# Kernel optimization log

Hardware: AMD Instinct MI355X
Metric: run time of the kernel (lower is better)

The kernel has to match this reference:

```python
import jax, jax.numpy as jnp
import numpy as np

B, T_ENC, T_DEC = 16, 256, 200
E, ATT, PRE, H, MEL, LOC, K = 512, 128, 256, 1024, 80, 32, 31


def setup_inputs() -> dict:
    key = jax.random.key(0)
    ks = jax.random.split(key, 20)
    s = lambda k, shape: jax.random.normal(k, shape, jnp.float32) * 0.02
    return dict(
        encoder_output=jax.random.normal(ks[0], (B, T_ENC, E), jnp.float32),
        padded_mels=jax.random.normal(ks[1], (B, T_DEC, MEL), jnp.float32),
        enc_proj_w=s(ks[2], (ATT, E)),
        lstm_proj_w=s(ks[3], (ATT, H)),
        loc_conv_w=s(ks[4], (LOC, 1, K)),
        loc_conv_b=jnp.zeros((LOC,), jnp.float32),
        loc_dense_w=s(ks[5], (ATT, LOC)),
        loc_dense_b=jnp.zeros((ATT,), jnp.float32),
        e_w=s(ks[6], (1, ATT)),
        e_b=jnp.zeros((1,), jnp.float32),
        prenet1_w=s(ks[7], (PRE, MEL)),
        prenet2_w=s(ks[8], (PRE, PRE)),
        w_ih0=s(ks[9], (4 * H, PRE + E)),
        w_hh0=s(ks[10], (4 * H, H)),
        b_ih0=jnp.zeros((4 * H,), jnp.float32),
        b_hh0=jnp.zeros((4 * H,), jnp.float32),
        w_ih1=s(ks[11], (4 * H, H)),
        w_hh1=s(ks[12], (4 * H, H)),
        b_ih1=jnp.zeros((4 * H,), jnp.float32),
        b_hh1=jnp.zeros((4 * H,), jnp.float32),
        proj_w=s(ks[13], (MEL, H + E)),
        proj_b=jnp.zeros((MEL,), jnp.float32),
        stop_w=s(ks[14], (1, H + E)),
        stop_b=jnp.zeros((1,), jnp.float32),
        text_lengths=jax.random.randint(ks[15], (B,), T_ENC // 2, T_ENC + 1),
    )


def _lstm_cell_zero(x, w_ih, b_ih, b_hh):
    # PyTorch LSTM cell with zero initial (h, c): h_prev contributes nothing
    # except the recurrent bias b_hh. Gate order: i, f, g, o.
    g = x @ w_ih.T + b_ih + b_hh
    i, f, gg, o = jnp.split(g, 4, axis=-1)
    c = jax.nn.sigmoid(i) * jnp.tanh(gg)  # f * c_prev == 0
    return jax.nn.sigmoid(o) * jnp.tanh(c)


def reference(encoder_output, padded_mels, enc_proj_w, lstm_proj_w, loc_conv_w,
              loc_conv_b, loc_dense_w, loc_dense_b, e_w, e_b, prenet1_w,
              prenet2_w, w_ih0, w_hh0, b_ih0, b_hh0, w_ih1, w_hh1, b_ih1,
              b_hh1, proj_w, proj_b, stop_w, stop_b, text_lengths):
    b, t_enc, _ = encoder_output.shape
    n_mel = padded_mels.shape[-1]
    h = w_hh0.shape[-1]
    pad = (loc_conv_w.shape[-1] - 1) // 2
    proc_enc = encoder_output @ enc_proj_w.T              # [B,Te,128]
    mask = jnp.arange(t_enc)[None, :] < text_lengths[:, None]
    # teacher forcing (ratio=1.0): prev mel at step t is padded_mels[:, t-1]
    prev_mels = jnp.concatenate(
        [jnp.zeros((b, 1, n_mel), padded_mels.dtype), padded_mels[:, :-1]],
        axis=1).transpose(1, 0, 2)                        # [Td,B,80]

    def step(carry, prev_mel):
        awc, h2 = carry                                   # [B,Te], [B,1024]
        # prenet (dropout omitted for a deterministic reference)
        x = jax.nn.relu(prev_mel @ prenet1_w.T)
        x = jax.nn.relu(x @ prenet2_w.T)                  # [B,256]
        # location-sensitive attention
        q = h2 @ lstm_proj_w.T                            # [B,128]
        loc = jax.lax.conv_general_dilated(
            awc[:, None, :], loc_conv_w, (1,), [(pad, pad)],
            dimension_numbers=('NCH', 'OIH', 'NCH')) + loc_conv_b[None, :, None]
        loc = jnp.einsum('bct,ac->bta', loc, loc_dense_w) + loc_dense_b
        en = jnp.tanh(q[:, None, :] + loc + proc_enc) @ e_w[0] + e_b[0]
        en = jnp.where(mask, en, -1e9)
        aw = jax.nn.softmax(en, axis=-1)                  # [B,Te]
        ctx = jnp.einsum('bt,bte->be', aw, encoder_output)  # [B,512]
        # 2-layer LSTM, state reset to zero every step (as in the original)
        li = jnp.concatenate([x, ctx], axis=-1)           # [B,768]
        h1 = _lstm_cell_zero(li, w_ih0, b_ih0, b_hh0)
        h2n = _lstm_cell_zero(h1, w_ih1, b_ih1, b_hh1)
        dec = jnp.concatenate([h2n, ctx], axis=-1)        # [B,1536]
        mel = dec @ proj_w.T + proj_b                     # [B,80]
        stop = (dec @ stop_w.T + stop_b)[:, 0]            # [B]
        return (awc + aw, h2n), (mel, stop)

    init = (jnp.zeros((b, t_enc), encoder_output.dtype),
            jnp.zeros((b, h), encoder_output.dtype))
    _, (mels, stops) = jax.lax.scan(step, init, prev_mels)
    return mels.transpose(1, 0, 2), stops.T               # [B,Td,80], [B,Td]
```

## Files before the change

kernel.cpp:

```cpp
#include <hip/hip_runtime.h>
#include <math.h>

#define NB   16
#define TE   256
#define TD   200
#define EE   512
#define ATT  128
#define PREN 256
#define HH   1024
#define NMEL 80
#define NLOC 32
#define KWW  31
#define PADW 15

#define OFF_X2   0
#define OFF_PE   (OFF_X2 + TD*NB*PREN)
#define OFF_AWC  (OFF_PE + NB*TE*ATT)
#define OFF_EN   (OFF_AWC + NB*TE)
#define OFF_Q    (OFF_EN + NB*TE)
#define OFF_CTX  (OFF_Q + NB*ATT)
#define OFF_H1   (OFF_CTX + NB*EE)
#define OFF_H2   (OFF_H1 + NB*HH)
#define OFF_BAR  (OFF_H2 + NB*HH)
#define BAR_U32  8192

#define ARR_G  0
#define ARR_L  4096

#define LW0_F4   (12*192)
#define LW1_F4   (12*256)
#define DYN_BYTES ((LW0_F4 + LW1_F4) * 16)

typedef float f4 __attribute__((ext_vector_type(4)));

__device__ __forceinline__ float sigmf(float x) { return 1.0f / (1.0f + expf(-x)); }
__device__ __forceinline__ float dot4(f4 a, f4 b) {
  return a.x*b.x + a.y*b.y + a.z*b.z + a.w*b.w;
}
__device__ __forceinline__ float red32(float v) {
  v += __shfl_down(v, 16, 32); v += __shfl_down(v, 8, 32);
  v += __shfl_down(v, 4, 32);  v += __shfl_down(v, 2, 32);
  v += __shfl_down(v, 1, 32);
  return v;
}

__device__ __forceinline__ unsigned ld_cg_u32(const unsigned* p) {
  unsigned r;
  asm volatile("global_load_dword %0, %1, off sc0 sc1\n\ts_waitcnt vmcnt(0)"
               : "=v"(r) : "v"(p) : "memory");
  return r;
}
__device__ __forceinline__ void st_cg_u32(unsigned* p, unsigned v) {
  asm volatile("global_store_dword %0, %1, off sc0 sc1" :: "v"(p), "v"(v) : "memory");
}
__device__ __forceinline__ float ld_cg_f32(const float* p) {
  float r;
  asm volatile("global_load_dword %0, %1, off sc0 sc1\n\ts_waitcnt vmcnt(0)"
               : "=v"(r) : "v"(p) : "memory");
  return r;
}
__device__ __forceinline__ void st_cg_f32(float* p, float v) {
  asm volatile("global_store_dword %0, %1, off sc0 sc1" :: "v"(p), "v"(v) : "memory");
}
__device__ __forceinline__ f4 ld_cg_f4(const f4* p) {
  f4 r;
  asm volatile("global_load_dwordx4 %0, %1, off sc0 sc1\n\ts_waitcnt vmcnt(0)"
               : "=v"(r) : "v"(p) : "memory");
  return r;
}
__device__ __forceinline__ void st_cg_f4(f4* p, f4 v) {
  asm volatile("global_store_dwordx4 %0, %1, off sc0 sc1" :: "v"(p), "v"(v) : "memory");
}
__device__ __forceinline__ void ld4_cg(f4& r0, f4& r1, f4& r2, f4& r3,
                                       const f4* a0, const f4* a1,
                                       const f4* a2, const f4* a3) {
  asm volatile(
    "global_load_dwordx4 %0, %4, off sc0 sc1\n\t"
    "global_load_dwordx4 %1, %5, off sc0 sc1\n\t"
    "global_load_dwordx4 %2, %6, off sc0 sc1\n\t"
    "global_load_dwordx4 %3, %7, off sc0 sc1\n\t"
    "s_waitcnt vmcnt(0)"
    : "=&v"(r0), "=&v"(r1), "=&v"(r2), "=&v"(r3)
    : "v"(a0), "v"(a1), "v"(a2), "v"(a3)
    : "memory");
}
__device__ __forceinline__ void ld8_cg(f4& r0, f4& r1, f4& r2, f4& r3,
                                       f4& r4, f4& r5, f4& r6, f4& r7,
                                       const f4* a0, const f4* a1, const f4* a2,
                                       const f4* a3, const f4* a4, const f4* a5,
                                       const f4* a6, const f4* a7) {
  asm volatile(
    "global_load_dwordx4 %0, %8, off sc0 sc1\n\t"
    "global_load_dwordx4 %1, %9, off sc0 sc1\n\t"
    "global_load_dwordx4 %2, %10, off sc0 sc1\n\t"
    "global_load_dwordx4 %3, %11, off sc0 sc1\n\t"
    "global_load_dwordx4 %4, %12, off sc0 sc1\n\t"
    "global_load_dwordx4 %5, %13, off sc0 sc1\n\t"
    "global_load_dwordx4 %6, %14, off sc0 sc1\n\t"
    "global_load_dwordx4 %7, %15, off sc0 sc1\n\t"
    "s_waitcnt vmcnt(0)"
    : "=&v"(r0), "=&v"(r1), "=&v"(r2), "=&v"(r3),
      "=&v"(r4), "=&v"(r5), "=&v"(r6), "=&v"(r7)
    : "v"(a0), "v"(a1), "v"(a2), "v"(a3),
      "v"(a4), "v"(a5), "v"(a6), "v"(a7)
    : "memory");
}

__device__ __forceinline__ void g_arrive(unsigned* bar, unsigned e) {
  __syncthreads();
  if (threadIdx.x == 0) st_cg_u32(bar + ARR_G + blockIdx.x * 16, e);
}
__device__ __forceinline__ void g_wait(unsigned* bar, unsigned e) {
  if (threadIdx.x < 256) {
    while (ld_cg_u32(bar + ARR_G + threadIdx.x * 16) < e) {}
  }
  __syncthreads();
}
__device__ __forceinline__ void l_arrive(unsigned* bar, unsigned e) {
  __syncthreads();
  if (threadIdx.x == 0) st_cg_u32(bar + ARR_L + blockIdx.x * 16, e);
}
__device__ __forceinline__ void l_wait(unsigned* bar, unsigned e, int b_grp) {
  if (threadIdx.x < 16) {
    while (ld_cg_u32(bar + ARR_L + (threadIdx.x * 16 + b_grp) * 16) < e) {}
  }
  __syncthreads();
}

__global__ void k_init(float* __restrict__ ws) {
  const int tid = threadIdx.x;
  float* awc = ws + OFF_AWC;
  float* qv  = ws + OFF_Q;
  unsigned* bar = (unsigned*)(ws + OFF_BAR);
  for (int i = tid; i < NB*TE; i += 256) st_cg_f32(awc + i, 0.0f);
  for (int i = tid; i < NB*ATT; i += 256) st_cg_f32(qv + i, 0.0f);
  for (int i = tid; i < BAR_U32; i += 256) st_cg_u32(bar + i, 0u);
}

__global__ void k_prenet(const float* __restrict__ mels,
                         const float* __restrict__ w1,
                         const float* __restrict__ w2,
                         float* __restrict__ x2) {
  const int t = blockIdx.x >> 4;
  const int b = blockIdx.x & 15;
  const int j = threadIdx.x;
  __shared__ float s_in[NMEL];
  __shared__ float s_x1[PREN];
  if (j < NMEL) s_in[j] = (t == 0) ? 0.0f : mels[(b*TD + (t-1))*NMEL + j];
  __syncthreads();
  float a1 = 0.0f;
  #pragma unroll 8
  for (int k = 0; k < NMEL; ++k) a1 += s_in[k] * w1[j*NMEL + k];
  s_x1[j] = fmaxf(a1, 0.0f);
  __syncthreads();
  float a2 = 0.0f;
  #pragma unroll 8
  for (int k = 0; k < PREN; ++k) a2 += s_x1[k] * w2[j*PREN + k];
  x2[(t*NB + b)*PREN + j] = fmaxf(a2, 0.0f);
}

__global__ void k_procenc(const float* __restrict__ enc,
                          const float* __restrict__ w,
                          float* __restrict__ pe) {
  const int bt = blockIdx.x;
  const int a = threadIdx.x;
  __shared__ float s_e[EE];
  for (int k = a; k < EE; k += 128) s_e[k] = enc[bt*EE + k];
  __syncthreads();
  float acc = 0.0f;
  #pragma unroll 8
  for (int k = 0; k < EE; ++k) acc += s_e[k] * w[a*EE + k];
  pe[bt*ATT + a] = acc;
}

__global__ void __launch_bounds__(512, 1) k_main(
    const float* __restrict__ enc,
    const float* __restrict__ lstm_proj_w,
    const float* __restrict__ loc_conv_w,
    const float* __restrict__ loc_conv_b,
    const float* __restrict__ loc_dense_w,
    const float* __restrict__ loc_dense_b,
    const float* __restrict__ e_w,
    const float* __restrict__ e_b,
    const float* __restrict__ w_ih0,
    const float* __restrict__ b_ih0,
    const float* __restrict__ b_hh0,
    const float* __restrict__ w_ih1,
    const float* __restrict__ b_ih1,
    const float* __restrict__ b_hh1,
    const float* __restrict__ proj_w,
    const float* __restrict__ proj_b,
    const float* __restrict__ stop_w,
    const float* __restrict__ stop_b,
    const int*   __restrict__ text_len,
    float* __restrict__ ws,
    float* __restrict__ out) {
  const int bid = blockIdx.x;
  const int tid = threadIdx.x;

  float* x2  = ws + OFF_X2;
  float* pe  = ws + OFF_PE;
  float* awc = ws + OFF_AWC;
  float* en  = ws + OFF_EN;
  float* qv  = ws + OFF_Q;
  float* ctx = ws + OFF_CTX;
  float* h1  = ws + OFF_H1;
  float* h2  = ws + OFF_H2;
  unsigned* bar = (unsigned*)(ws + OFF_BAR);

  __shared__ __align__(16) float s_ldw[NLOC*ATT];
  __shared__ float s_awc[64];
  __shared__ float s_loc[16*33];
  __shared__ float s_red[16];
  __shared__ float s_aw[256];
  __shared__ __align__(16) float s_dec[HH+EE];
  __shared__ float s_b0[12], s_b1[12];
  extern __shared__ __align__(16) float dynlds[];
  f4* lw0 = (f4*)dynlds;
  f4* lw1 = ((f4*)dynlds) + LW0_F4;

  const int b_grp = bid & 15;
  const int sub   = bid >> 4;
  const int h0    = bid * 4;

  for (int i = tid; i < NLOC*ATT; i += 512) {
    int c = i >> 7, a = i & 127;
    s_ldw[i] = loc_dense_w[a*NLOC + c];
  }
  if (tid < 12) {
    int g = tid >> 2, h = tid & 3;
    int gr = (g == 0 ? 0 : (g == 1 ? 2048 : 3072)) + h0 + h;
    s_b0[tid] = b_ih0[gr] + b_hh0[gr];
    s_b1[tid] = b_ih1[gr] + b_hh1[gr];
  }
  {
    const f4* w0_4 = (const f4*)w_ih0;
    const f4* w1_4 = (const f4*)w_ih1;
    for (int i = tid; i < LW0_F4; i += 512) {
      int r = i / 192, c = i - r*192;
      int g = r >> 2, h = r & 3;
      int grow = (g == 0 ? 0 : (g == 1 ? 2048 : 3072)) + h0 + h;
      lw0[i] = w0_4[grow*192 + c];
    }
    for (int i = tid; i < LW1_F4; i += 512) {
      int r = i >> 8, c = i & 255;
      int g = r >> 2, h = r & 3;
      int grow = (g == 0 ? 0 : (g == 1 ? 2048 : 3072)) + h0 + h;
      lw1[i] = w1_4[grow*256 + c];
    }
  }
  const int   lenb = text_len[b_grp];
  const float eb0  = e_b[0];

  const int tl = tid >> 5;
  const int j  = tid & 31;
  float lcw_r[KWW];
  #pragma unroll
  for (int k = 0; k < KWW; ++k) lcw_r[k] = loc_conv_w[j*KWW + k];
  const float lcb_r = loc_conv_b[j];
  const f4 db_r = *(const f4*)(loc_dense_b + 4*j);
  const f4 ew_r = *(const f4*)(e_w + 4*j);
  const f4 pe_r = *(const f4*)(pe + (size_t)(b_grp*TE + sub*16 + tl)*ATT + 4*j);
  const f4 ps_r = pe_r + db_r;
  const int e4i = tid >> 6;
  const int ts  = tid & 63;
  f4 encr[4];
  {
    const f4* enc4 = (const f4*)(enc + (size_t)b_grp*TE*EE);
    #pragma unroll
    for (int i = 0; i < 4; ++i)
      encr[i] = enc4[(size_t)(ts + 64*i)*(EE/4) + sub*8 + e4i];
  }
  const int pb = tid >> 5;
  const int kc = tid & 31;
  __syncthreads();

  unsigned eg = 0, el = 0;

  for (int t = 0; t < TD; ++t) {
    f4 pre;
    {
      if (tid >= 128 && tid < 176) {
        const int i = tid - 128;
        const int g = sub*16 - PADW + i;
        s_awc[i] = (i < 46 && g >= 0 && g < TE) ? ld_cg_f32(awc + b_grp*TE + g)
                                                : 0.0f;
      }
      __syncthreads();
      float cv = lcb_r;
      #pragma unroll
      for (int k = 0; k < KWW; ++k) cv += s_awc[tl + k] * lcw_r[k];
      s_loc[tl*33 + j] = cv;
      __syncthreads();
      f4 d4 = (f4){0.f, 0.f, 0.f, 0.f};
      #pragma unroll 8
      for (int c = 0; c < NLOC; ++c) {
        const float lv = s_loc[tl*33 + c];
        const f4 w4 = ((const f4*)s_ldw)[c*32 + j];
        d4.x += lv*w4.x; d4.y += lv*w4.y; d4.z += lv*w4.z; d4.w += lv*w4.w;
      }
      pre = ps_r + d4;
    }
    l_wait(bar, el, b_grp);
    {
      const f4 q4 = ld_cg_f4((const f4*)qv + b_grp*32 + j);
      float acc = tanhf(pre.x+q4.x)*ew_r.x + tanhf(pre.y+q4.y)*ew_r.y
                + tanhf(pre.z+q4.z)*ew_r.z + tanhf(pre.w+q4.w)*ew_r.w;
      acc = red32(acc);
      if (j == 0) {
        float evv = acc + eb0;
        const int tt = sub*16 + tl;
        if (tt >= lenb) evv = -1e9f;
        st_cg_f32(en + b_grp*TE + tt, evv);
      }
    }
    l_arrive(bar, ++el);
    l_wait(bar, el, b_grp);
    {
      float evv = 0.f, p = 0.f;
      if (tid < 256) {
        evv = ld_cg_f32(en + b_grp*TE + tid);
        float m = evv;
        #pragma unroll
        for (int d = 32; d > 0; d >>= 1) m = fmaxf(m, __shfl_xor(m, d));
        if ((tid & 63) == 0) s_red[tid >> 6] = m;
      }
      __syncthreads();
      const float mx = fmaxf(fmaxf(s_red[0], s_red[1]), fmaxf(s_red[2], s_red[3]));
      if (tid < 256) {
        p = expf(evv - mx);
        float sm = p;
        #pragma unroll
        for (int d = 32; d > 0; d >>= 1) sm += __shfl_xor(sm, d);
        if ((tid & 63) == 0) s_red[8 + (tid >> 6)] = sm;
      }
      __syncthreads();
      const float inv = 1.0f / (s_red[8] + s_red[9] + s_red[10] + s_red[11]);
      if (tid < 256) {
        const float aw = p * inv;
        s_aw[tid] = aw;
        if (sub == 0) {
          const float old = ld_cg_f32(awc + b_grp*TE + tid);
          st_cg_f32(awc + b_grp*TE + tid, old + aw);
        }
      }
      __syncthreads();
      f4 a4 = (f4){0.f, 0.f, 0.f, 0.f};
      #pragma unroll
      for (int i = 0; i < 4; ++i) {
        const float awv = s_aw[ts + 64*i];
        a4.x += awv*encr[i].x; a4.y += awv*encr[i].y;
        a4.z += awv*encr[i].z; a4.w += awv*encr[i].w;
      }
      #pragma unroll
      for (int d = 32; d > 0; d >>= 1) {
        a4.x += __shfl_down(a4.x, d);
        a4.y += __shfl_down(a4.y, d);
        a4.z += __shfl_down(a4.z, d);
        a4.w += __shfl_down(a4.w, d);
      }
      if (ts == 0) st_cg_f4((f4*)ctx + b_grp*(EE/4) + sub*8 + e4i, a4);
    }
    g_arrive(bar, ++eg);
    float acc[12];
    {
      #pragma unroll
      for (int r = 0; r < 12; ++r) acc[r] = 0.0f;
      const f4* x4p = (const f4*)(x2 + (size_t)(t*NB + pb)*PREN);
      #pragma unroll
      for (int i = 0; i < 2; ++i) {
        const int kf = kc + 32*i;
        const f4 xv = x4p[kf];
        #pragma unroll
        for (int r = 0; r < 12; ++r) acc[r] += dot4(xv, lw0[r*192 + kf]);
      }
    }
    g_wait(bar, eg);
    {
      const f4* c4p = (const f4*)(ctx + pb*EE);
      f4 cv0, cv1, cv2, cv3;
      ld4_cg(cv0, cv1, cv2, cv3, c4p+kc, c4p+kc+32, c4p+kc+64, c4p+kc+96);
      #pragma unroll
      for (int r = 0; r < 12; ++r) {
        acc[r] += dot4(cv0, lw0[r*192 + 64 + kc]);
        acc[r] += dot4(cv1, lw0[r*192 + 64 + kc + 32]);
        acc[r] += dot4(cv2, lw0[r*192 + 64 + kc + 64]);
        acc[r] += dot4(cv3, lw0[r*192 + 64 + kc + 96]);
      }
      #pragma unroll
      for (int r = 0; r < 12; ++r) acc[r] = red32(acc[r]);
      if (kc == 0) {
        f4 hv;
        #pragma unroll
        for (int h = 0; h < 4; ++h) {
          const float gi = acc[h]   + s_b0[h];
          const float gg = acc[4+h] + s_b0[4+h];
          const float go = acc[8+h] + s_b0[8+h];
          const float c = sigmf(gi) * tanhf(gg);
          hv[h] = sigmf(go) * tanhf(c);
        }
        st_cg_f4((f4*)h1 + pb*(HH/4) + bid, hv);
      }
    }
    g_arrive(bar, ++eg);
    g_wait(bar, eg);
    {
      #pragma unroll
      for (int r = 0; r < 12; ++r) acc[r] = 0.0f;
      const f4* h4p = (const f4*)(h1 + pb*HH);
      f4 hv0, hv1, hv2, hv3, hv4, hv5, hv6, hv7;
      ld8_cg(hv0, hv1, hv2, hv3, hv4, hv5, hv6, hv7,
             h4p+kc, h4p+kc+32, h4p+kc+64, h4p+kc+96,
             h4p+kc+128, h4p+kc+160, h4p+kc+192, h4p+kc+224);
      #pragma unroll
      for (int r = 0; r < 12; ++r) {
        acc[r] += dot4(hv0, lw1[r*256 + kc]);
        acc[r] += dot4(hv1, lw1[r*256 + kc + 32]);
        acc[r] += dot4(hv2, lw1[r*256 + kc + 64]);
        acc[r] += dot4(hv3, lw1[r*256 + kc + 96]);
        acc[r] += dot4(hv4, lw1[r*256 + kc + 128]);
        acc[r] += dot4(hv5, lw1[r*256 + kc + 160]);
        acc[r] += dot4(hv6, lw1[r*256 + kc + 192]);
        acc[r] += dot4(hv7, lw1[r*256 + kc + 224]);
      }
      #pragma unroll
      for (int r = 0; r < 12; ++r) acc[r] = red32(acc[r]);
      if (kc == 0) {
        f4 hv;
        #pragma unroll
        for (int h = 0; h < 4; ++h) {
          const float gi = acc[h]   + s_b1[h];
          const float gg = acc[4+h] + s_b1[4+h];
          const float go = acc[8+h] + s_b1[8+h];
          const float c = sigmf(gi) * tanhf(gg);
          hv[h] = sigmf(go) * tanhf(c);
        }
        st_cg_f4((f4*)h2 + pb*(HH/4) + bid, hv);
      }
    }
    g_arrive(bar, ++eg);
    if (tid >= 256 && tid < 384)
      ((f4*)s_dec)[tid] = ld_cg_f4((const f4*)ctx + b_grp*(EE/4) + (tid - 256));
    g_wait(bar, eg);
    {
      if (tid < 256)
        ((f4*)s_dec)[tid] = ld_cg_f4((const f4*)h2 + b_grp*(HH/4) + tid);
      __syncthreads();
      const int ol = tid >> 5;
      const int kq = tid & 31;
      const f4* s4 = (const f4*)s_dec;
      if (sub < 8) {
        const int a = sub*16 + ol;
        const f4* w4 = (const f4*)(lstm_proj_w + (size_t)a*HH);
        float a2 = 0.0f;
        #pragma unroll
        for (int i = 0; i < 8; ++i) a2 += dot4(s4[kq + 32*i], w4[kq + 32*i]);
        a2 = red32(a2);
        if (kq == 0) st_cg_f32(qv + b_grp*ATT + a, a2);
      } else {
        const int m = (sub - 8)*11 + ol;
        if (ol < 11 && m < 81) {
          const float* wrow = (m < NMEL) ? (proj_w + (size_t)m*(HH+EE)) : stop_w;
          const f4* w4 = (const f4*)wrow;
          float a2 = 0.0f;
          #pragma unroll
          for (int i = 0; i < 12; ++i) a2 += dot4(s4[kq + 32*i], w4[kq + 32*i]);
          a2 = red32(a2);
          if (kq == 0) {
            if (m < NMEL) out[(b_grp*TD + t)*NMEL + m] = a2 + proj_b[m];
            else          out[NB*TD*NMEL + b_grp*TD + t] = a2 + stop_b[0];
          }
        }
      }
    }
    l_arrive(bar, ++el);
  }
}

extern "C" void kernel_launch(void* const* d_in, const int* in_sizes, int n_in,
                              void* d_out, int out_size, void* d_ws, size_t ws_size,
                              hipStream_t stream) {
  (void)in_sizes; (void)n_in; (void)out_size; (void)ws_size;
  const float* enc         = (const float*)d_in[0];
  const float* mels        = (const float*)d_in[1];
  const float* enc_proj_w  = (const float*)d_in[2];
  const float* lstm_proj_w = (const float*)d_in[3];
  const float* loc_conv_w  = (const float*)d_in[4];
  const float* loc_conv_b  = (const float*)d_in[5];
  const float* loc_dense_w = (const float*)d_in[6];
  const float* loc_dense_b = (const float*)d_in[7];
  const float* e_w         = (const float*)d_in[8];
  const float* e_b         = (const float*)d_in[9];
  const float* prenet1_w   = (const float*)d_in[10];
  const float* prenet2_w   = (const float*)d_in[11];
  const float* w_ih0       = (const float*)d_in[12];
  const float* b_ih0       = (const float*)d_in[14];
  const float* b_hh0       = (const float*)d_in[15];
  const float* w_ih1       = (const float*)d_in[16];
  const float* b_ih1       = (const float*)d_in[18];
  const float* b_hh1       = (const float*)d_in[19];
  const float* proj_w      = (const float*)d_in[20];
  const float* proj_b      = (const float*)d_in[21];
  const float* stop_w      = (const float*)d_in[22];
  const float* stop_b      = (const float*)d_in[23];
  const int*   text_len    = (const int*)d_in[24];
  float* ws  = (float*)d_ws;
  float* out = (float*)d_out;

  static int attr_set = 0;
  if (!attr_set) {
    hipFuncSetAttribute((const void*)k_main,
                        hipFuncAttributeMaxDynamicSharedMemorySize, DYN_BYTES);
    attr_set = 1;
  }

  k_init<<<dim3(1), dim3(256), 0, stream>>>(ws);
  k_prenet<<<dim3(TD*NB), dim3(256), 0, stream>>>(mels, prenet1_w, prenet2_w, ws + OFF_X2);
  k_procenc<<<dim3(NB*TE), dim3(128), 0, stream>>>(enc, enc_proj_w, ws + OFF_PE);

  k_main<<<dim3(256), dim3(512), DYN_BYTES, stream>>>(
      enc, lstm_proj_w, loc_conv_w, loc_conv_b, loc_dense_w, loc_dense_b,
      e_w, e_b, w_ih0, b_ih0, b_hh0, w_ih1, b_ih1, b_hh1,
      proj_w, proj_b, stop_w, stop_b, text_len, ws, out);
}
```

Before: 4.471 ms.

## Replace grid barriers with step-tagged data records and fp16 packed hidden states

```diff
diff --git a/kernel.cpp b/kernel.cpp
--- a/kernel.cpp
+++ b/kernel.cpp
@@ -1,4 +1,5 @@
 #include <hip/hip_runtime.h>
+#include <hip/hip_fp16.h>
 #include <math.h>
 
 #define NB   16
@@ -16,20 +17,17 @@
 #define OFF_X2   0
 #define OFF_PE   (OFF_X2 + TD*NB*PREN)
 #define OFF_AWC  (OFF_PE + NB*TE*ATT)
-#define OFF_EN   (OFF_AWC + NB*TE)
-#define OFF_Q    (OFF_EN + NB*TE)
-#define OFF_CTX  (OFF_Q + NB*ATT)
-#define OFF_H1   (OFF_CTX + NB*EE)
-#define OFF_H2   (OFF_H1 + NB*HH)
-#define OFF_BAR  (OFF_H2 + NB*HH)
-#define BAR_U32  8192
-
-#define ARR_G  0
-#define ARR_L  4096
-
-#define LW0_F4   (12*192)
+#define OFF_ENR  (OFF_AWC + NB*TE)
+#define OFF_QVR  (OFF_ENR + NB*16*6*4)
+#define OFF_CTR  (OFF_QVR + NB*16*2*4)
+#define OFF_H1R  (OFF_CTR + NB*176*4)
+#define OFF_H2R  (OFF_H1R + NB*256*4)
+#define OFF_END  (OFF_H2R + NB*256*4)
+
+#define LW0X_F4  (12*64)
+#define LW0C_F4  (12*177)
 #define LW1_F4   (12*256)
-#define DYN_BYTES ((LW0_F4 + LW1_F4) * 16)
+#define DYN_BYTES ((LW0X_F4 + LW0C_F4 + LW1_F4) * 16)
 
 typedef float f4 __attribute__((ext_vector_type(4)));
 
@@ -43,16 +41,22 @@
   v += __shfl_down(v, 1, 32);
   return v;
 }
-
-__device__ __forceinline__ unsigned ld_cg_u32(const unsigned* p) {
-  unsigned r;
-  asm volatile("global_load_dword %0, %1, off sc0 sc1\n\ts_waitcnt vmcnt(0)"
-               : "=v"(r) : "v"(p) : "memory");
-  return r;
-}
-__device__ __forceinline__ void st_cg_u32(unsigned* p, unsigned v) {
-  asm volatile("global_store_dword %0, %1, off sc0 sc1" :: "v"(p), "v"(v) : "memory");
-}
+__device__ __forceinline__ float red64(float v) {
+  v += __shfl_down(v, 32); v += __shfl_down(v, 16); v += __shfl_down(v, 8);
+  v += __shfl_down(v, 4);  v += __shfl_down(v, 2);  v += __shfl_down(v, 1);
+  return v;
+}
+__device__ __forceinline__ float h2f_lo(unsigned u) {
+  return __half2float(__ushort_as_half((unsigned short)(u & 0xffffu)));
+}
+__device__ __forceinline__ float h2f_hi(unsigned u) {
+  return __half2float(__ushort_as_half((unsigned short)(u >> 16)));
+}
+__device__ __forceinline__ unsigned pack2h(float a, float b) {
+  return (unsigned)__half_as_ushort(__float2half_rn(a)) |
+         ((unsigned)__half_as_ushort(__float2half_rn(b)) << 16);
+}
+
 __device__ __forceinline__ float ld_cg_f32(const float* p) {
   float r;
   asm volatile("global_load_dword %0, %1, off sc0 sc1\n\ts_waitcnt vmcnt(0)"
@@ -71,17 +75,19 @@
 __device__ __forceinline__ void st_cg_f4(f4* p, f4 v) {
   asm volatile("global_store_dwordx4 %0, %1, off sc0 sc1" :: "v"(p), "v"(v) : "memory");
 }
-__device__ __forceinline__ void ld4_cg(f4& r0, f4& r1, f4& r2, f4& r3,
-                                       const f4* a0, const f4* a1,
-                                       const f4* a2, const f4* a3) {
+__device__ __forceinline__ void ld6_cg(f4& r0, f4& r1, f4& r2, f4& r3, f4& r4, f4& r5,
+                                       const f4* a0, const f4* a1, const f4* a2,
+                                       const f4* a3, const f4* a4, const f4* a5) {
   asm volatile(
-    "global_load_dwordx4 %0, %4, off sc0 sc1\n\t"
-    "global_load_dwordx4 %1, %5, off sc0 sc1\n\t"
-    "global_load_dwordx4 %2, %6, off sc0 sc1\n\t"
-    "global_load_dwordx4 %3, %7, off sc0 sc1\n\t"
+    "global_load_dwordx4 %0, %6, off sc0 sc1\n\t"
+    "global_load_dwordx4 %1, %7, off sc0 sc1\n\t"
+    "global_load_dwordx4 %2, %8, off sc0 sc1\n\t"
+    "global_load_dwordx4 %3, %9, off sc0 sc1\n\t"
+    "global_load_dwordx4 %4, %10, off sc0 sc1\n\t"
+    "global_load_dwordx4 %5, %11, off sc0 sc1\n\t"
     "s_waitcnt vmcnt(0)"
-    : "=&v"(r0), "=&v"(r1), "=&v"(r2), "=&v"(r3)
-    : "v"(a0), "v"(a1), "v"(a2), "v"(a3)
+    : "=&v"(r0), "=&v"(r1), "=&v"(r2), "=&v"(r3), "=&v"(r4), "=&v"(r5)
+    : "v"(a0), "v"(a1), "v"(a2), "v"(a3), "v"(a4), "v"(a5)
     : "memory");
 }
 __device__ __forceinline__ void ld8_cg(f4& r0, f4& r1, f4& r2, f4& r3,
@@ -106,35 +112,14 @@
     : "memory");
 }
 
-__device__ __forceinline__ void g_arrive(unsigned* bar, unsigned e) {
-  __syncthreads();
-  if (threadIdx.x == 0) st_cg_u32(bar + ARR_G + blockIdx.x * 16, e);
-}
-__device__ __forceinline__ void g_wait(unsigned* bar, unsigned e) {
-  if (threadIdx.x < 256) {
-    while (ld_cg_u32(bar + ARR_G + threadIdx.x * 16) < e) {}
-  }
-  __syncthreads();
-}
-__device__ __forceinline__ void l_arrive(unsigned* bar, unsigned e) {
-  __syncthreads();
-  if (threadIdx.x == 0) st_cg_u32(bar + ARR_L + blockIdx.x * 16, e);
-}
-__device__ __forceinline__ void l_wait(unsigned* bar, unsigned e, int b_grp) {
-  if (threadIdx.x < 16) {
-    while (ld_cg_u32(bar + ARR_L + (threadIdx.x * 16 + b_grp) * 16) < e) {}
-  }
-  __syncthreads();
-}
-
 __global__ void k_init(float* __restrict__ ws) {
-  const int tid = threadIdx.x;
+  const int gid = blockIdx.x * 256 + threadIdx.x;
   float* awc = ws + OFF_AWC;
-  float* qv  = ws + OFF_Q;
-  unsigned* bar = (unsigned*)(ws + OFF_BAR);
-  for (int i = tid; i < NB*TE; i += 256) st_cg_f32(awc + i, 0.0f);
-  for (int i = tid; i < NB*ATT; i += 256) st_cg_f32(qv + i, 0.0f);
-  for (int i = tid; i < BAR_U32; i += 256) st_cg_u32(bar + i, 0u);
+  for (int i = gid; i < NB*TE; i += 32*256) st_cg_f32(awc + i, 0.0f);
+  f4* recs = (f4*)(ws + OFF_ENR);
+  const int nrec = (OFF_END - OFF_ENR) / 4;
+  const f4 z = (f4){0.f, 0.f, 0.f, 0.f};
+  for (int i = gid; i < nrec; i += 32*256) st_cg_f4(recs + i, z);
 }
 
 __global__ void k_prenet(const float* __restrict__ mels,
@@ -201,23 +186,28 @@
   float* x2  = ws + OFF_X2;
   float* pe  = ws + OFF_PE;
   float* awc = ws + OFF_AWC;
-  float* en  = ws + OFF_EN;
-  float* qv  = ws + OFF_Q;
-  float* ctx = ws + OFF_CTX;
-  float* h1  = ws + OFF_H1;
-  float* h2  = ws + OFF_H2;
-  unsigned* bar = (unsigned*)(ws + OFF_BAR);
+  f4* en_rec = (f4*)(ws + OFF_ENR);
+  f4* qv_rec = (f4*)(ws + OFF_QVR);
+  f4* ct_rec = (f4*)(ws + OFF_CTR);
+  f4* h1_rec = (f4*)(ws + OFF_H1R);
+  f4* h2_rec = (f4*)(ws + OFF_H2R);
 
   __shared__ __align__(16) float s_ldw[NLOC*ATT];
   __shared__ float s_awc[64];
   __shared__ float s_loc[16*33];
   __shared__ float s_red[16];
+  __shared__ float s_en[256];
   __shared__ float s_aw[256];
+  __shared__ float s_entmp[16];
+  __shared__ float s_ctmp[32];
+  __shared__ float s_qtmp[8];
+  __shared__ __align__(16) float s_q[ATT];
   __shared__ __align__(16) float s_dec[HH+EE];
   __shared__ float s_b0[12], s_b1[12];
   extern __shared__ __align__(16) float dynlds[];
-  f4* lw0 = (f4*)dynlds;
-  f4* lw1 = ((f4*)dynlds) + LW0_F4;
+  f4* lw0x = (f4*)dynlds;
+  f4* lw0c = lw0x + LW0X_F4;
+  f4* lw1  = lw0c + LW0C_F4;
 
   const int b_grp = bid & 15;
   const int sub   = bid >> 4;
@@ -236,11 +226,25 @@
   {
     const f4* w0_4 = (const f4*)w_ih0;
     const f4* w1_4 = (const f4*)w_ih1;
-    for (int i = tid; i < LW0_F4; i += 512) {
-      int r = i / 192, c = i - r*192;
+    for (int i = tid; i < LW0X_F4; i += 512) {
+      int r = i >> 6, c = i & 63;
       int g = r >> 2, h = r & 3;
       int grow = (g == 0 ? 0 : (g == 1 ? 2048 : 3072)) + h0 + h;
-      lw0[i] = w0_4[grow*192 + c];
+      lw0x[i] = w0_4[grow*192 + c];
+    }
+    for (int i = tid; i < LW0C_F4; i += 512) {
+      int r = i / 177, e = i - r*177;
+      f4 v = (f4){0.f, 0.f, 0.f, 0.f};
+      if (e < 176) {
+        int g = r >> 2, h = r & 3;
+        int grow = (g == 0 ? 0 : (g == 1 ? 2048 : 3072)) + h0 + h;
+        int s = e / 11, rr = e - s*11;
+        int base = s*32 + 3*rr;
+        if (base + 0 < s*32 + 32) v.x = w_ih0[(size_t)grow*768 + 256 + base + 0];
+        if (3*rr + 1 < 32)        v.y = w_ih0[(size_t)grow*768 + 256 + base + 1];
+        if (3*rr + 2 < 32)        v.z = w_ih0[(size_t)grow*768 + 256 + base + 2];
+      }
+      lw0c[i] = v;
     }
     for (int i = tid; i < LW1_F4; i += 512) {
       int r = i >> 8, c = i & 255;
@@ -273,11 +277,17 @@
   }
   const int pb = tid >> 5;
   const int kc = tid & 31;
+  int ridx[6], widx[6];
+  #pragma unroll
+  for (int i = 0; i < 6; ++i) {
+    if (kc < 16) { ridx[i] = kc*6 + i; widx[i] = ridx[i]; }
+    else if (i < 5) { ridx[i] = 96 + (kc-16)*5 + i; widx[i] = ridx[i]; }
+    else { ridx[i] = 0; widx[i] = 176; }
+  }
   __syncthreads();
 
-  unsigned eg = 0, el = 0;
-
   for (int t = 0; t < TD; ++t) {
+    const unsigned tg = (unsigned)(t + 1);
     f4 pre;
     {
       if (tid >= 128 && tid < 176) {
@@ -301,9 +311,18 @@
       }
       pre = ps_r + d4;
     }
-    l_wait(bar, el, b_grp);
     {
-      const f4 q4 = ld_cg_f4((const f4*)qv + b_grp*32 + j);
+      if (tid < 32) {
+        const f4* qp = qv_rec + (b_grp*16 + (tid >> 1))*2 + (tid & 1);
+        f4 r;
+        do { r = ld_cg_f4(qp); } while (__float_as_uint(r.z) != (unsigned)t);
+        const unsigned u0 = __float_as_uint(r.x), u1 = __float_as_uint(r.y);
+        const int base = (tid >> 1)*8 + (tid & 1)*4;
+        s_q[base+0] = h2f_lo(u0); s_q[base+1] = h2f_hi(u0);
+        s_q[base+2] = h2f_lo(u1); s_q[base+3] = h2f_hi(u1);
+      }
+      __syncthreads();
+      const f4 q4 = *(const f4*)(s_q + 4*j);
       float acc = tanhf(pre.x+q4.x)*ew_r.x + tanhf(pre.y+q4.y)*ew_r.y
                 + tanhf(pre.z+q4.z)*ew_r.z + tanhf(pre.w+q4.w)*ew_r.w;
       acc = red32(acc);
@@ -311,15 +330,49 @@
         float evv = acc + eb0;
         const int tt = sub*16 + tl;
         if (tt >= lenb) evv = -1e9f;
-        st_cg_f32(en + b_grp*TE + tt, evv);
-      }
-    }
-    l_arrive(bar, ++el);
-    l_wait(bar, el, b_grp);
+        s_entmp[tl] = evv;
+      }
+      __syncthreads();
+      if (tid < 6) {
+        f4 r = (f4){0.f, 0.f, 0.f, __uint_as_float(tg)};
+        const int base = 3*tid;
+        r.x = s_entmp[base];
+        if (base + 1 < 16) r.y = s_entmp[base+1];
+        if (base + 2 < 16) r.z = s_entmp[base+2];
+        st_cg_f4(en_rec + (b_grp*16 + sub)*6 + tid, r);
+      }
+      if (t > 0 && sub >= 8) {
+        const int m = (sub - 8)*11 + tl;
+        if (tl < 11 && m < 81) {
+          const float* wrow = (m < NMEL) ? (proj_w + (size_t)m*(HH+EE)) : stop_w;
+          const f4* w4 = (const f4*)wrow;
+          const f4* s4 = (const f4*)s_dec;
+          float a2 = 0.0f;
+          #pragma unroll
+          for (int i = 0; i < 12; ++i) a2 += dot4(s4[j + 32*i], w4[j + 32*i]);
+          a2 = red32(a2);
+          if (j == 0) {
+            if (m < NMEL) out[(b_grp*TD + (t-1))*NMEL + m] = a2 + proj_b[m];
+            else          out[NB*TD*NMEL + b_grp*TD + (t-1)] = a2 + stop_b[0];
+          }
+        }
+      }
+    }
     {
+      if (tid < 96) {
+        const int si = tid / 6, r = tid - si*6;
+        const f4* ep = en_rec + (b_grp*16 + si)*6 + r;
+        f4 v;
+        do { v = ld_cg_f4(ep); } while (__float_as_uint(v.w) != tg);
+        const int base = si*16 + 3*r;
+        s_en[base] = v.x;
+        if (3*r + 1 < 16) s_en[base+1] = v.y;
+        if (3*r + 2 < 16) s_en[base+2] = v.z;
+      }
+      __syncthreads();
       float evv = 0.f, p = 0.f;
       if (tid < 256) {
-        evv = ld_cg_f32(en + b_grp*TE + tid);
+        evv = s_en[tid];
         float m = evv;
         #pragma unroll
         for (int d = 32; d > 0; d >>= 1) m = fmaxf(m, __shfl_xor(m, d));
@@ -352,18 +405,23 @@
         a4.x += awv*encr[i].x; a4.y += awv*encr[i].y;
         a4.z += awv*encr[i].z; a4.w += awv*encr[i].w;
       }
-      #pragma unroll
-      for (int d = 32; d > 0; d >>= 1) {
-        a4.x += __shfl_down(a4.x, d);
-        a4.y += __shfl_down(a4.y, d);
-        a4.z += __shfl_down(a4.z, d);
-        a4.w += __shfl_down(a4.w, d);
-      }
-      if (ts == 0) st_cg_f4((f4*)ctx + b_grp*(EE/4) + sub*8 + e4i, a4);
-    }
-    g_arrive(bar, ++eg);
-    float acc[12];
+      a4.x = red64(a4.x); a4.y = red64(a4.y); a4.z = red64(a4.z); a4.w = red64(a4.w);
+      if (ts == 0) {
+        s_ctmp[e4i*4+0] = a4.x; s_ctmp[e4i*4+1] = a4.y;
+        s_ctmp[e4i*4+2] = a4.z; s_ctmp[e4i*4+3] = a4.w;
+      }
+      __syncthreads();
+      if (tid < 11) {
+        f4 r = (f4){0.f, 0.f, 0.f, __uint_as_float(tg)};
+        const int base = 3*tid;
+        r.x = s_ctmp[base];
+        if (base + 1 < 32) r.y = s_ctmp[base+1];
+        if (base + 2 < 32) r.z = s_ctmp[base+2];
+        st_cg_f4(ct_rec + b_grp*176 + sub*11 + tid, r);
+      }
+    }
     {
+      float acc[12];
       #pragma unroll
       for (int r = 0; r < 12; ++r) acc[r] = 0.0f;
       const f4* x4p = (const f4*)(x2 + (size_t)(t*NB + pb)*PREN);
@@ -372,108 +430,144 @@
         const int kf = kc + 32*i;
         const f4 xv = x4p[kf];
         #pragma unroll
-        for (int r = 0; r < 12; ++r) acc[r] += dot4(xv, lw0[r*192 + kf]);
-      }
-    }
-    g_wait(bar, eg);
-    {
-      const f4* c4p = (const f4*)(ctx + pb*EE);
-      f4 cv0, cv1, cv2, cv3;
-      ld4_cg(cv0, cv1, cv2, cv3, c4p+kc, c4p+kc+32, c4p+kc+64, c4p+kc+96);
+        for (int r = 0; r < 12; ++r) acc[r] += dot4(xv, lw0x[r*64 + kf]);
+      }
+      const f4* cr = ct_rec + pb*176;
+      f4 c0, c1, c2, c3, c4, c5;
+      for (;;) {
+        ld6_cg(c0, c1, c2, c3, c4, c5,
+               cr+ridx[0], cr+ridx[1], cr+ridx[2], cr+ridx[3], cr+ridx[4], cr+ridx[5]);
+        if (__float_as_uint(c0.w) == tg && __float_as_uint(c1.w) == tg &&
+            __float_as_uint(c2.w) == tg && __float_as_uint(c3.w) == tg &&
+            __float_as_uint(c4.w) == tg && __float_as_uint(c5.w) == tg) break;
+      }
       #pragma unroll
       for (int r = 0; r < 12; ++r) {
-        acc[r] += dot4(cv0, lw0[r*192 + 64 + kc]);
-        acc[r] += dot4(cv1, lw0[r*192 + 64 + kc + 32]);
-        acc[r] += dot4(cv2, lw0[r*192 + 64 + kc + 64]);
-        acc[r] += dot4(cv3, lw0[r*192 + 64 + kc + 96]);
+        acc[r] += dot4(c0, lw0c[r*177 + widx[0]]);
+        acc[r] += dot4(c1, lw0c[r*177 + widx[1]]);
+        acc[r] += dot4(c2, lw0c[r*177 + widx[2]]);
+        acc[r] += dot4(c3, lw0c[r*177 + widx[3]]);
+        acc[r] += dot4(c4, lw0c[r*177 + widx[4]]);
+        acc[r] += dot4(c5, lw0c[r*177 + widx[5]]);
       }
       #pragma unroll
       for (int r = 0; r < 12; ++r) acc[r] = red32(acc[r]);
       if (kc == 0) {
-        f4 hv;
+        float hv[4];
         #pragma unroll
         for (int h = 0; h < 4; ++h) {
           const float gi = acc[h]   + s_b0[h];
           const float gg = acc[4+h] + s_b0[4+h];
           const float go = acc[8+h] + s_b0[8+h];
-          const float c = sigmf(gi) * tanhf(gg);
-          hv[h] = sigmf(go) * tanhf(c);
+          hv[h] = sigmf(go) * tanhf(sigmf(gi) * tanhf(gg));
         }
-        st_cg_f4((f4*)h1 + pb*(HH/4) + bid, hv);
-      }
-    }
-    g_arrive(bar, ++eg);
-    g_wait(bar, eg);
+        f4 r = (f4){__uint_as_float(pack2h(hv[0], hv[1])),
+                    __uint_as_float(pack2h(hv[2], hv[3])),
+                    __uint_as_float(tg), 0.f};
+        st_cg_f4(h1_rec + pb*256 + bid, r);
+      }
+    }
     {
+      float acc[12];
       #pragma unroll
       for (int r = 0; r < 12; ++r) acc[r] = 0.0f;
-      const f4* h4p = (const f4*)(h1 + pb*HH);
-      f4 hv0, hv1, hv2, hv3, hv4, hv5, hv6, hv7;
-      ld8_cg(hv0, hv1, hv2, hv3, hv4, hv5, hv6, hv7,
-             h4p+kc, h4p+kc+32, h4p+kc+64, h4p+kc+96,
-             h4p+kc+128, h4p+kc+160, h4p+kc+192, h4p+kc+224);
-      #pragma unroll
-      for (int r = 0; r < 12; ++r) {
-        acc[r] += dot4(hv0, lw1[r*256 + kc]);
-        acc[r] += dot4(hv1, lw1[r*256 + kc + 32]);
-        acc[r] += dot4(hv2, lw1[r*256 + kc + 64]);
-        acc[r] += dot4(hv3, lw1[r*256 + kc + 96]);
-        acc[r] += dot4(hv4, lw1[r*256 + kc + 128]);
-        acc[r] += dot4(hv5, lw1[r*256 + kc + 160]);
-        acc[r] += dot4(hv6, lw1[r*256 + kc + 192]);
-        acc[r] += dot4(hv7, lw1[r*256 + kc + 224]);
+      const f4* hr = h1_rec + pb*256;
+      f4 v0, v1, v2, v3, v4, v5, v6, v7;
+      for (;;) {
+        ld8_cg(v0, v1, v2, v3, v4, v5, v6, v7,
+               hr+kc, hr+kc+32, hr+kc+64, hr+kc+96,
+               hr+kc+128, hr+kc+160, hr+kc+192, hr+kc+224);
+        if (__float_as_uint(v0.z) == tg && __float_as_uint(v1.z) == tg &&
+            __float_as_uint(v2.z) == tg && __float_as_uint(v3.z) == tg &&
+            __float_as_uint(v4.z) == tg && __float_as_uint(v5.z) == tg &&
+            __float_as_uint(v6.z) == tg && __float_as_uint(v7.z) == tg) break;
+      }
+      f4 recs[8] = {v0, v1, v2, v3, v4, v5, v6, v7};
+      #pragma unroll
+      for (int i = 0; i < 8; ++i) {
+        const unsigned u0 = __float_as_uint(recs[i].x);
+        const unsigned u1 = __float_as_uint(recs[i].y);
+        const float f0 = h2f_lo(u0), f1 = h2f_hi(u0);
+        const float f2 = h2f_lo(u1), f3 = h2f_hi(u1);
+        const int blk = kc + 32*i;
+        #pragma unroll
+        for (int r = 0; r < 12; ++r) {
+          const f4 w = lw1[r*256 + blk];
+          acc[r] += f0*w.x + f1*w.y + f2*w.z + f3*w.w;
+        }
       }
       #pragma unroll
       for (int r = 0; r < 12; ++r) acc[r] = red32(acc[r]);
       if (kc == 0) {
-        f4 hv;
+        float hv[4];
         #pragma unroll
         for (int h = 0; h < 4; ++h) {
           const float gi = acc[h]   + s_b1[h];
           const float gg = acc[4+h] + s_b1[4+h];
           const float go = acc[8+h] + s_b1[8+h];
-          const float c = sigmf(gi) * tanhf(gg);
-          hv[h] = sigmf(go) * tanhf(c);
+          hv[h] = sigmf(go) * tanhf(sigmf(gi) * tanhf(gg));
         }
-        st_cg_f4((f4*)h2 + pb*(HH/4) + bid, hv);
-      }
-    }
-    g_arrive(bar, ++eg);
-    if (tid >= 256 && tid < 384)
-      ((f4*)s_dec)[tid] = ld_cg_f4((const f4*)ctx + b_grp*(EE/4) + (tid - 256));
-    g_wait(bar, eg);
+        f4 r = (f4){__uint_as_float(pack2h(hv[0], hv[1])),
+                    __uint_as_float(pack2h(hv[2], hv[3])),
+                    __uint_as_float(tg), 0.f};
+        st_cg_f4(h2_rec + pb*256 + bid, r);
+      }
+    }
     {
-      if (tid < 256)
-        ((f4*)s_dec)[tid] = ld_cg_f4((const f4*)h2 + b_grp*(HH/4) + tid);
-      __syncthreads();
-      const int ol = tid >> 5;
-      const int kq = tid & 31;
+      if (tid < 256) {
+        const f4* hp = h2_rec + b_grp*256 + tid;
+        f4 r;
+        do { r = ld_cg_f4(hp); } while (__float_as_uint(r.z) != tg);
+        const unsigned u0 = __float_as_uint(r.x), u1 = __float_as_uint(r.y);
+        s_dec[4*tid+0] = h2f_lo(u0); s_dec[4*tid+1] = h2f_hi(u0);
+        s_dec[4*tid+2] = h2f_lo(u1); s_dec[4*tid+3] = h2f_hi(u1);
+      } else if (tid < 432) {
+        const int i = tid - 256;
+        const f4* cp = ct_rec + b_grp*176 + i;
+        f4 r;
+        do { r = ld_cg_f4(cp); } while (__float_as_uint(r.w) != tg);
+        const int si = i / 11, rr = i - si*11;
+        const int base = HH + si*32 + 3*rr;
+        s_dec[base] = r.x;
+        if (3*rr + 1 < 32) s_dec[base+1] = r.y;
+        if (3*rr + 2 < 32) s_dec[base+2] = r.z;
+      }
+      __syncthreads();
+      const int row = tid >> 6;
+      const int kq  = tid & 63;
+      const int a   = sub*8 + row;
       const f4* s4 = (const f4*)s_dec;
-      if (sub < 8) {
-        const int a = sub*16 + ol;
-        const f4* w4 = (const f4*)(lstm_proj_w + (size_t)a*HH);
-        float a2 = 0.0f;
-        #pragma unroll
-        for (int i = 0; i < 8; ++i) a2 += dot4(s4[kq + 32*i], w4[kq + 32*i]);
-        a2 = red32(a2);
-        if (kq == 0) st_cg_f32(qv + b_grp*ATT + a, a2);
-      } else {
-        const int m = (sub - 8)*11 + ol;
-        if (ol < 11 && m < 81) {
-          const float* wrow = (m < NMEL) ? (proj_w + (size_t)m*(HH+EE)) : stop_w;
-          const f4* w4 = (const f4*)wrow;
-          float a2 = 0.0f;
-          #pragma unroll
-          for (int i = 0; i < 12; ++i) a2 += dot4(s4[kq + 32*i], w4[kq + 32*i]);
-          a2 = red32(a2);
-          if (kq == 0) {
-            if (m < NMEL) out[(b_grp*TD + t)*NMEL + m] = a2 + proj_b[m];
-            else          out[NB*TD*NMEL + b_grp*TD + t] = a2 + stop_b[0];
-          }
-        }
-      }
-    }
-    l_arrive(bar, ++el);
+      const f4* w4 = (const f4*)(lstm_proj_w + (size_t)a*HH);
+      float a2 = 0.0f;
+      #pragma unroll
+      for (int i = 0; i < 4; ++i) a2 += dot4(s4[kq + 64*i], w4[kq + 64*i]);
+      a2 = red64(a2);
+      if (kq == 0) s_qtmp[row] = a2;
+      __syncthreads();
+      if (tid < 2) {
+        f4 r = (f4){__uint_as_float(pack2h(s_qtmp[4*tid],   s_qtmp[4*tid+1])),
+                    __uint_as_float(pack2h(s_qtmp[4*tid+2], s_qtmp[4*tid+3])),
+                    __uint_as_float(tg), 0.f};
+        st_cg_f4(qv_rec + (b_grp*16 + sub)*2 + tid, r);
+      }
+    }
+  }
+  __syncthreads();
+  if (sub >= 8) {
+    const int m = (sub - 8)*11 + tl;
+    if (tl < 11 && m < 81) {
+      const float* wrow = (m < NMEL) ? (proj_w + (size_t)m*(HH+EE)) : stop_w;
+      const f4* w4 = (const f4*)wrow;
+      const f4* s4 = (const f4*)s_dec;
+      float a2 = 0.0f;
+      #pragma unroll
+      for (int i = 0; i < 12; ++i) a2 += dot4(s4[j + 32*i], w4[j + 32*i]);
+      a2 = red32(a2);
+      if (j == 0) {
+        if (m < NMEL) out[(b_grp*TD + (TD-1))*NMEL + m] = a2 + proj_b[m];
+        else          out[NB*TD*NMEL + b_grp*TD + (TD-1)] = a2 + stop_b[0];
+      }
+    }
   }
 }
 
@@ -514,7 +608,7 @@
     attr_set = 1;
   }
 
-  k_init<<<dim3(1), dim3(256), 0, stream>>>(ws);
+  k_init<<<dim3(32), dim3(256), 0, stream>>>(ws);
   k_prenet<<<dim3(TD*NB), dim3(256), 0, stream>>>(mels, prenet1_w, prenet2_w, ws + OFF_X2);
   k_procenc<<<dim3(NB*TE), dim3(128), 0, stream>>>(enc, enc_proj_w, ws + OFF_PE);
 
```

Result: slower. 6.892 ms (+54.1%).
